# Performance work log

Measured on AMD Instinct MI355X. Metric: run time of the kernel, lower is better.

The kernel has to match this reference:

```python
import jax, jax.numpy as jnp
import numpy as np

N_NODES = 50000
N_EDGES = 800000
NFEAT, NHID, IN_HEAD, NCLASS, OUT_HEAD = 256, 16, 8, 47, 1
NEG_SLOPE = 0.2


def setup_inputs() -> dict:
    key = jax.random.key(0)
    ks = jax.random.split(key, 10)
    x = jax.random.normal(ks[0], (N_NODES, NFEAT), dtype=jnp.float32)
    edge_index = jax.random.randint(ks[1], (2, N_EDGES), 0, N_NODES, dtype=jnp.int64)
    W1 = jax.random.normal(ks[2], (NFEAT, IN_HEAD * NHID), dtype=jnp.float32) * 0.06
    a1_src = jax.random.normal(ks[3], (IN_HEAD, NHID), dtype=jnp.float32) * 0.25
    a1_dst = jax.random.normal(ks[4], (IN_HEAD, NHID), dtype=jnp.float32) * 0.25
    b1 = jax.random.normal(ks[5], (IN_HEAD * NHID,), dtype=jnp.float32) * 0.02
    W2 = jax.random.normal(ks[6], (IN_HEAD * NHID, NCLASS), dtype=jnp.float32) * 0.09
    a2_src = jax.random.normal(ks[7], (OUT_HEAD, NCLASS), dtype=jnp.float32) * 0.15
    a2_dst = jax.random.normal(ks[8], (OUT_HEAD, NCLASS), dtype=jnp.float32) * 0.15
    b2 = jax.random.normal(ks[9], (NCLASS,), dtype=jnp.float32) * 0.02
    return {"x": x, "edge_index": edge_index, "W1": W1, "a1_src": a1_src,
            "a1_dst": a1_dst, "b1": b1, "W2": W2, "a2_src": a2_src,
            "a2_dst": a2_dst, "b2": b2}


def _gat_layer(x, W, a_src, a_dst, b, src, dst, n_nodes, concat):
    # x: [N, F_in]; W: [F_in, H*C]; a_*: [H, C]
    H, C = a_src.shape
    h = (x @ W).reshape(n_nodes, H, C)                        # [N, H, C]
    # per-node partial attention logits, then gather per edge
    s_src = jnp.einsum('nhc,hc->nh', h, a_src)                # [N, H]
    s_dst = jnp.einsum('nhc,hc->nh', h, a_dst)                # [N, H]
    e = jax.nn.leaky_relu(s_src[src] + s_dst[dst], NEG_SLOPE) # [E, H]
    # segment softmax over destination node
    m = jax.ops.segment_max(e, dst, num_segments=n_nodes)     # [N, H]
    ex = jnp.exp(e - m[dst])
    denom = jax.ops.segment_sum(ex, dst, num_segments=n_nodes)
    alpha = ex / (denom[dst] + 1e-16)                         # [E, H]
    # weighted message aggregation (scatter-add)
    msg = alpha[:, :, None] * h[src]                          # [E, H, C]
    out = jax.ops.segment_sum(msg, dst, num_segments=n_nodes) # [N, H, C]
    out = out.reshape(n_nodes, H * C) if concat else out.mean(axis=1)
    return out + b


def reference(x, edge_index, W1, a1_src, a1_dst, b1, W2, a2_src, a2_dst, b2):
    n = x.shape[0]
    # PyG GATConv default: add self-loops
    loops = jnp.arange(n, dtype=edge_index.dtype)
    src = jnp.concatenate([edge_index[0], loops])
    dst = jnp.concatenate([edge_index[1], loops])
    # eval mode: dropout is identity
    h = _gat_layer(x, W1, a1_src, a1_dst, b1, src, dst, n, concat=True)
    h = jax.nn.elu(h)
    out = _gat_layer(h, W2, a2_src, a2_dst, b2, src, dst, n, concat=False)
    return jax.nn.log_softmax(out, axis=1)
```

## Files before the change

### kernel.cpp

```cpp
#include <hip/hip_runtime.h>
#include <hip/hip_fp16.h>

#define N_NODES 50000
#define N_EDGES 800000
#define E2 (N_EDGES + N_NODES)

#define BSHIFT 6
#define BMASK 63
#define NBUCK 782
#define EPB 4096
#define NBLKC 208

typedef _Float16 h8v __attribute__((ext_vector_type(8)));
typedef float f4v __attribute__((ext_vector_type(4)));


__global__ __launch_bounds__(256) void k_hist(const int* __restrict__ ei,
        int* __restrict__ gh, const float* __restrict__ W1, _Float16* __restrict__ W1T) {
    if (blockIdx.x == NBLKC) {
        for (int i = threadIdx.x; i < 128 * 256; i += 256) {
            int c = i >> 8, k = i & 255;
            W1T[i] = (_Float16)W1[k * 128 + c];
        }
        return;
    }
    __shared__ int h[NBUCK];
    int tid = threadIdx.x;
    for (int b = tid; b < NBUCK; b += 256) h[b] = 0;
    __syncthreads();
    int base = blockIdx.x * EPB;
    for (int i = tid; i < EPB; i += 256) {
        int e = base + i;
        if (e < E2) {
            int dst = (e < N_EDGES) ? ei[N_EDGES + e] : (e - N_EDGES);
            atomicAdd(&h[dst >> BSHIFT], 1);
        }
    }
    __syncthreads();
    for (int b = tid; b < NBUCK; b += 256) gh[blockIdx.x * NBUCK + b] = h[b];
}

__global__ __launch_bounds__(256) void k_colscan(int* __restrict__ gh,
                                                 int* __restrict__ tot) {
    int wave = threadIdx.x >> 6, lane = threadIdx.x & 63;
    int b = blockIdx.x * 4 + wave;
    if (b >= NBUCK) return;
    int carry = 0;
    for (int c = 0; c < NBLKC; c += 64) {
        int k = c + lane;
        int v = (k < NBLKC) ? gh[k * NBUCK + b] : 0;
        int x = v;
        #pragma unroll
        for (int o = 1; o < 64; o <<= 1) { int y = __shfl_up(x, o); if (lane >= o) x += y; }
        if (k < NBLKC) gh[k * NBUCK + b] = carry + x - v;
        carry += __shfl(x, 63);
    }
    if (lane == 0) tot[b] = carry;
}

__global__ __launch_bounds__(1024) void k_btot(const int* __restrict__ tot,
        int* __restrict__ boff, const float* __restrict__ W2, float* __restrict__ W2p) {
    int t = threadIdx.x;
    for (int i = t; i < 128 * 48; i += 1024) {
        int k = i / 48, c = i - k * 48;
        W2p[i] = (c < 47) ? W2[k * 47 + c] : 0.f;
    }
    int v = (t < NBUCK) ? tot[t] : 0;
    __shared__ int ws[16];
    int lane = t & 63, w = t >> 6;
    int x = v;
    #pragma unroll
    for (int o = 1; o < 64; o <<= 1) { int y = __shfl_up(x, o); if (lane >= o) x += y; }
    if (lane == 63) ws[w] = x;
    __syncthreads();
    if (t == 0) {
        #pragma unroll
        for (int j = 1; j < 16; ++j) ws[j] += ws[j - 1];
    }
    __syncthreads();
    int add = (w == 0) ? 0 : ws[w - 1];
    int excl = add + x - v;
    if (t < NBUCK) boff[t] = excl;
    if (t == NBUCK - 1) boff[NBUCK] = excl + v;
}

__global__ __launch_bounds__(256) void k_place(const int* __restrict__ ei,
        const int* __restrict__ gh, const int* __restrict__ boff,
        unsigned int* __restrict__ brec) {
    __shared__ int sbase[NBUCK];
    __shared__ int cnt[NBUCK];
    int tid = threadIdx.x;
    for (int b = tid; b < NBUCK; b += 256) {
        sbase[b] = boff[b] + gh[blockIdx.x * NBUCK + b];
        cnt[b] = 0;
    }
    __syncthreads();
    int base = blockIdx.x * EPB;
    for (int i = tid; i < EPB; i += 256) {
        int e = base + i;
        if (e < E2) {
            int src, dst;
            if (e < N_EDGES) { src = ei[e]; dst = ei[N_EDGES + e]; }
            else             { src = dst = e - N_EDGES; }
            int b = dst >> BSHIFT;
            int r = atomicAdd(&cnt[b], 1);
            brec[sbase[b] + r] = ((unsigned int)(dst & BMASK) << 16) | (unsigned int)src;
        }
    }
}

__global__ __launch_bounds__(256) void k_finalize(const unsigned int* __restrict__ brec,
        const int* __restrict__ boff, unsigned short* __restrict__ csr_src,
        int* __restrict__ offs) {
    int B = blockIdx.x;
    int tid = threadIdx.x;
    int base = boff[B];
    int total = boff[B + 1] - base;
    __shared__ int hist[64], cur[64];
    __shared__ unsigned short stage[2048];
    if (tid < 64) hist[tid] = 0;
    __syncthreads();
    const unsigned int* bp = brec + base;
    for (int i = tid; i < total; i += 256) atomicAdd(&hist[bp[i] >> 16], 1);
    __syncthreads();
    if (tid < 64) {
        int v = hist[tid];
        int x = v;
        #pragma unroll
        for (int o = 1; o < 64; o <<= 1) { int y = __shfl_up(x, o); if (tid >= o) x += y; }
        int excl = x - v;
        cur[tid] = excl;
        int n = B * 64 + tid;
        if (n < N_NODES) offs[n] = base + excl;
    }
    if (B == NBUCK - 1 && tid == 0) offs[N_NODES] = boff[NBUCK];
    __syncthreads();
    if (total <= 2048) {
        for (int i = tid; i < total; i += 256) {
            unsigned int r = bp[i];
            int p = atomicAdd(&cur[r >> 16], 1);
            stage[p] = (unsigned short)(r & 0xFFFFu);
        }
        __syncthreads();
        for (int i = tid; i < total; i += 256) csr_src[base + i] = stage[i];
    } else {
        for (int i = tid; i < total; i += 256) {
            unsigned int r = bp[i];
            int p = atomicAdd(&cur[r >> 16], 1);
            csr_src[base + p] = (unsigned short)(r & 0xFFFFu);
        }
    }
}


__global__ __launch_bounds__(128) void k_gemm1(const float* __restrict__ x,
        const _Float16* __restrict__ W1T, _Float16* __restrict__ h1h) {
    int lane = threadIdx.x & 63;
    int wv = threadIdx.x >> 6;
    int rowbase = blockIdx.x * 64 + wv * 32;
    int r0 = lane & 15;
    int kg = lane >> 4;
    f4v acc[2][8];
    #pragma unroll
    for (int i = 0; i < 2; ++i)
        #pragma unroll
        for (int j = 0; j < 8; ++j) acc[i][j] = (f4v)0.f;

    #pragma unroll 1
    for (int kt = 0; kt < 256; kt += 32) {
        h8v a[2];
        #pragma unroll
        for (int rf = 0; rf < 2; ++rf) {
            int row = rowbase + rf * 16 + r0;
            if (row >= N_NODES) row = N_NODES - 1;
            const float* ap = x + (size_t)row * 256 + kt + kg * 8;
            float4 lo = *(const float4*)ap;
            float4 hi = *(const float4*)(ap + 4);
            h8v t;
            t[0] = (_Float16)lo.x; t[1] = (_Float16)lo.y;
            t[2] = (_Float16)lo.z; t[3] = (_Float16)lo.w;
            t[4] = (_Float16)hi.x; t[5] = (_Float16)hi.y;
            t[6] = (_Float16)hi.z; t[7] = (_Float16)hi.w;
            a[rf] = t;
        }
        #pragma unroll
        for (int cf = 0; cf < 8; ++cf) {
            h8v b = *(const h8v*)(W1T + (size_t)(cf * 16 + r0) * 256 + kt + kg * 8);
            acc[0][cf] = __builtin_amdgcn_mfma_f32_16x16x32_f16(a[0], b, acc[0][cf], 0, 0, 0);
            acc[1][cf] = __builtin_amdgcn_mfma_f32_16x16x32_f16(a[1], b, acc[1][cf], 0, 0, 0);
        }
    }
    #pragma unroll
    for (int rf = 0; rf < 2; ++rf) {
        #pragma unroll
        for (int r = 0; r < 4; ++r) {
            int row = rowbase + rf * 16 + kg * 4 + r;
            if (row < N_NODES) {
                _Float16* orow = h1h + (size_t)row * 128 + r0;
                #pragma unroll
                for (int cf = 0; cf < 8; ++cf)
                    orow[cf * 16] = (_Float16)acc[rf][cf][r];
            }
        }
    }
}


__global__ void k_logits1(const __half* __restrict__ h1h,
                          const float* __restrict__ a1s, const float* __restrict__ a1d,
                          float* __restrict__ s1s, float* __restrict__ s1d) {
    int idx = blockIdx.x * blockDim.x + threadIdx.x;
    if (idx >= N_NODES * 8) return;
    int n = idx >> 3, h = idx & 7;
    const __half2* hp2 = (const __half2*)(h1h + (size_t)n * 128 + h * 16);
    float ss = 0.f, sd = 0.f;
    #pragma unroll
    for (int c2 = 0; c2 < 8; ++c2) {
        float2 v = __half22float2(hp2[c2]);
        ss += v.x * a1s[h * 16 + 2 * c2] + v.y * a1s[h * 16 + 2 * c2 + 1];
        sd += v.x * a1d[h * 16 + 2 * c2] + v.y * a1d[h * 16 + 2 * c2 + 1];
    }
    s1s[idx] = ss;
    s1d[idx] = sd;
}


__global__ __launch_bounds__(256) void k_agg1(const __half* __restrict__ h1h,
        const float* __restrict__ s1s, const float* __restrict__ s1d,
        const int* __restrict__ offs, const unsigned short* __restrict__ csr_src,
        const float* __restrict__ b1, __half* __restrict__ h2o) {
    int wave = threadIdx.x >> 6;
    int lane = threadIdx.x & 63;
    int n = blockIdx.x * 4 + wave;
    int beg = offs[n];
    int deg = offs[n + 1] - beg;

    int h = lane & 7;
    int slot = lane >> 3;
    int grp = lane >> 4;
    int cidx = lane & 15;
    int hc = cidx >> 1;
    float sdh = s1d[n * 8 + h];

    float dsum = 0.f;
    float acc[8] = {0.f, 0.f, 0.f, 0.f, 0.f, 0.f, 0.f, 0.f};
    for (int chunk = 0; chunk < deg; chunk += 16) {
        int i0 = chunk + slot;
        int i1 = chunk + 8 + slot;
        int e0 = csr_src[beg + ((i0 < deg) ? i0 : (deg - 1))];
        int e1 = csr_src[beg + ((i1 < deg) ? i1 : (deg - 1))];
        float a0 = 0.f, a1 = 0.f;
        if (i0 < deg) {
            float e = s1s[e0 * 8 + h] + sdh;
            e = (e > 0.f) ? e : 0.2f * e;
            a0 = __expf(e);
            dsum += a0;
        }
        if (i1 < deg) {
            float e = s1s[e1 * 8 + h] + sdh;
            e = (e > 0.f) ? e : 0.2f * e;
            a1 = __expf(e);
            dsum += a1;
        }
        int   s0 = __shfl(e0, grp * 8);       float w0 = __shfl(a0, grp * 8 + hc);
        int   s1 = __shfl(e0, (4 + grp) * 8); float w1 = __shfl(a0, (4 + grp) * 8 + hc);
        int   s2 = __shfl(e1, grp * 8);       float w2 = __shfl(a1, grp * 8 + hc);
        int   s3 = __shfl(e1, (4 + grp) * 8); float w3 = __shfl(a1, (4 + grp) * 8 + hc);
        h8v v0 = *(const h8v*)(h1h + (size_t)s0 * 128 + cidx * 8);
        h8v v1 = *(const h8v*)(h1h + (size_t)s1 * 128 + cidx * 8);
        h8v v2 = *(const h8v*)(h1h + (size_t)s2 * 128 + cidx * 8);
        h8v v3 = *(const h8v*)(h1h + (size_t)s3 * 128 + cidx * 8);
        #pragma unroll
        for (int j = 0; j < 8; ++j) acc[j] += w0 * (float)v0[j];
        #pragma unroll
        for (int j = 0; j < 8; ++j) acc[j] += w1 * (float)v1[j];
        #pragma unroll
        for (int j = 0; j < 8; ++j) acc[j] += w2 * (float)v2[j];
        #pragma unroll
        for (int j = 0; j < 8; ++j) acc[j] += w3 * (float)v3[j];
    }
    dsum += __shfl_xor(dsum, 8);
    dsum += __shfl_xor(dsum, 16);
    dsum += __shfl_xor(dsum, 32);
    float rd = 1.f / __shfl(dsum, hc);
    #pragma unroll
    for (int j = 0; j < 8; ++j) {
        acc[j] += __shfl_xor(acc[j], 16);
        acc[j] += __shfl_xor(acc[j], 32);
    }
    int c0 = cidx * 8 + grp * 2;
    float va = acc[grp * 2] * rd + b1[c0];
    va = (va > 0.f) ? va : (__expf(va) - 1.f);
    float vb = acc[grp * 2 + 1] * rd + b1[c0 + 1];
    vb = (vb > 0.f) ? vb : (__expf(vb) - 1.f);
    *(__half2*)(h2o + (size_t)n * 128 + c0) = __floats2half2_rn(va, vb);
}


__global__ __launch_bounds__(256) void k_gemm2(const __half* __restrict__ h2,
        const float* __restrict__ W2p,
        const float* __restrict__ a2s, const float* __restrict__ a2d,
        __half* __restrict__ g2h, float* __restrict__ s2s, float* __restrict__ s2d) {
    int n = blockIdx.x * 256 + threadIdx.x;
    bool valid = (n < N_NODES);
    int nn = valid ? n : (N_NODES - 1);
    const __half2* hrow = (const __half2*)(h2 + (size_t)nn * 128);
    float4 acc[12];
    #pragma unroll
    for (int j = 0; j < 12; ++j) acc[j] = make_float4(0.f, 0.f, 0.f, 0.f);
    #pragma unroll 1
    for (int k = 0; k < 128; k += 4) {
        float2 h01 = __half22float2(hrow[k / 2]);
        float2 h23 = __half22float2(hrow[k / 2 + 1]);
        float hk[4] = {h01.x, h01.y, h23.x, h23.y};
        #pragma unroll
        for (int kk = 0; kk < 4; ++kk) {
            const float* wrow = W2p + (size_t)(k + kk) * 48;
            #pragma unroll
            for (int j = 0; j < 12; ++j) {
                float4 wv = *(const float4*)(wrow + j * 4);
                acc[j].x += hk[kk] * wv.x;
                acc[j].y += hk[kk] * wv.y;
                acc[j].z += hk[kk] * wv.z;
                acc[j].w += hk[kk] * wv.w;
            }
        }
    }
    float vs = 0.f, vd = 0.f;
    #pragma unroll
    for (int j = 0; j < 12; ++j) {
        int c = j * 4;
        vs += acc[j].x * a2s[c + 0]; vd += acc[j].x * a2d[c + 0];
        vs += acc[j].y * a2s[c + 1]; vd += acc[j].y * a2d[c + 1];
        vs += acc[j].z * a2s[c + 2]; vd += acc[j].z * a2d[c + 2];
        if (j < 11) { vs += acc[j].w * a2s[c + 3]; vd += acc[j].w * a2d[c + 3]; }
    }
    if (valid) {
        __half2* orow = (__half2*)(g2h + (size_t)n * 48);
        #pragma unroll
        for (int j = 0; j < 12; ++j) {
            orow[j * 2 + 0] = __floats2half2_rn(acc[j].x, acc[j].y);
            orow[j * 2 + 1] = __floats2half2_rn(acc[j].z, acc[j].w);
        }
        s2s[n] = vs;
        s2d[n] = vd;
    }
}


__global__ __launch_bounds__(256) void k_agg2(const __half* __restrict__ g2h,
        const float* __restrict__ s2s, const float* __restrict__ s2d,
        const int* __restrict__ offs, const unsigned short* __restrict__ csr_src,
        const float* __restrict__ b2, float* __restrict__ outp) {
    int wave = threadIdx.x >> 6, lane = threadIdx.x & 63;
    int n = blockIdx.x * 4 + wave;
    int beg = offs[n];
    int deg = offs[n + 1] - beg;
    float sdn = s2d[n];
    int c = (lane < 47) ? lane : 47;

    float dsum = 0.f;
    float acc = 0.f;
    for (int chunk = 0; chunk < deg; chunk += 64) {
        int i = chunk + lane;
        int esrc = csr_src[beg + ((i < deg) ? i : (deg - 1))];
        float aN = 0.f;
        if (i < deg) {
            float e = s2s[esrc] + sdn;
            e = (e > 0.f) ? e : 0.2f * e;
            aN = __expf(e);
            dsum += aN;
        }
        int lim = deg - chunk; if (lim > 64) lim = 64;
        for (int g = 0; g < lim; g += 8) {
            int   srcs[8];
            float as[8];
            #pragma unroll
            for (int s = 0; s < 8; ++s) {
                srcs[s] = __shfl(esrc, g + s);
                as[s]   = __shfl(aN, g + s);
            }
            __half v[8];
            #pragma unroll
            for (int s = 0; s < 8; ++s) v[s] = g2h[(size_t)srcs[s] * 48 + c];
            #pragma unroll
            for (int s = 0; s < 8; ++s) acc += as[s] * __half2float(v[s]);
        }
    }
    #pragma unroll
    for (int o = 32; o; o >>= 1) dsum += __shfl_xor(dsum, o);
    acc *= 1.f / dsum;

    float l = (lane < 47) ? acc + b2[lane] : -1e30f;
    float rm = l;
    #pragma unroll
    for (int o = 32; o; o >>= 1) rm = fmaxf(rm, __shfl_xor(rm, o));
    float p = (lane < 47) ? __expf(l - rm) : 0.f;
    float ps = p;
    #pragma unroll
    for (int o = 32; o; o >>= 1) ps += __shfl_xor(ps, o);
    float lse = rm + __logf(ps);
    if (lane < 47) outp[(size_t)n * 47 + lane] = l - lse;
}


extern "C" void kernel_launch(void* const* d_in, const int* in_sizes, int n_in,
                              void* d_out, int out_size, void* d_ws, size_t ws_size,
                              hipStream_t stream) {
    const float* x   = (const float*)d_in[0];
    const int*   ei  = (const int*)d_in[1];
    const float* W1  = (const float*)d_in[2];
    const float* a1s = (const float*)d_in[3];
    const float* a1d = (const float*)d_in[4];
    const float* b1  = (const float*)d_in[5];
    const float* W2  = (const float*)d_in[6];
    const float* a2s = (const float*)d_in[7];
    const float* a2d = (const float*)d_in[8];
    const float* b2  = (const float*)d_in[9];
    float* outp = (float*)d_out;

    char* ws = (char*)d_ws;
    size_t off = 0;
    auto alloc = [&](size_t bytes) -> void* {
        void* p = ws + off;
        off += (bytes + 255) & ~(size_t)255;
        return p;
    };
    int* gh      = (int*)alloc((size_t)NBLKC * NBUCK * 4);
    int* tot     = (int*)alloc((size_t)NBUCK * 4);
    int* boff    = (int*)alloc((size_t)(NBUCK + 1) * 4);
    unsigned int* brec = (unsigned int*)alloc((size_t)E2 * 4);
    unsigned short* csr_src = (unsigned short*)alloc((size_t)E2 * 2);
    int* offs    = (int*)alloc((size_t)(N_NODES + 1) * 4);
    __half* h1h  = (__half*)alloc((size_t)N_NODES * 128 * 2);
    float* s1s   = (float*)alloc((size_t)N_NODES * 8 * 4);
    float* s1d   = (float*)alloc((size_t)N_NODES * 8 * 4);
    __half* h2h  = (__half*)alloc((size_t)N_NODES * 128 * 2);
    __half* g2h  = (__half*)alloc((size_t)N_NODES * 48 * 2);
    float* s2s   = (float*)alloc((size_t)N_NODES * 4);
    float* s2d   = (float*)alloc((size_t)N_NODES * 4);
    float* W2p   = (float*)alloc((size_t)128 * 48 * 4);
    _Float16* W1T = (_Float16*)alloc((size_t)128 * 256 * 2);

    (void)in_sizes; (void)n_in; (void)out_size; (void)ws_size;

    k_hist<<<NBLKC + 1, 256, 0, stream>>>(ei, gh, W1, W1T);
    k_colscan<<<(NBUCK + 3) / 4, 256, 0, stream>>>(gh, tot);
    k_btot<<<1, 1024, 0, stream>>>(tot, boff, W2, W2p);
    k_place<<<NBLKC, 256, 0, stream>>>(ei, gh, boff, brec);
    k_finalize<<<NBUCK, 256, 0, stream>>>(brec, boff, csr_src, offs);

    k_gemm1<<<(N_NODES + 63) / 64, 128, 0, stream>>>(x, W1T, (_Float16*)h1h);
    k_logits1<<<(N_NODES * 8 + 255) / 256, 256, 0, stream>>>(h1h, a1s, a1d, s1s, s1d);
    k_agg1<<<N_NODES / 4, 256, 0, stream>>>(h1h, s1s, s1d, offs, csr_src, b1, h2h);

    k_gemm2<<<(N_NODES + 255) / 256, 256, 0, stream>>>(h2h, W2p, a2s, a2d, g2h, s2s, s2d);
    k_agg2<<<N_NODES / 4, 256, 0, stream>>>(g2h, s2s, s2d, offs, csr_src, b2, outp);
}
```

Baseline: 178.4 us.

## Fuse logits into GEMM1, merge bucket scan kernels, halve edges per histogram block

Computes the layer-1 attention logits inside the GEMM1 epilogue using cross-lane shuffle reductions over the fp32 accumulators, which removes the separate k_logits1 kernel and its re-read of h1h. The bucket-total scan and the W2 padding move into k_colscan's last-arriving block, found with an atomic counter and threadfence, so the 1024-thread k_btot launch goes away. The counting-sort block size is halved (NBLKC doubled), which spreads the histogram and place work over more blocks but doubles the per-block histogram rows the column scan must walk. Logits now come from fp32 accumulators instead of fp16-rounded values, so they differ slightly in precision.

```diff
diff --git a/kernel.cpp b/kernel.cpp
--- a/kernel.cpp
+++ b/kernel.cpp
@@ -8,16 +8,18 @@
 #define BSHIFT 6
 #define BMASK 63
 #define NBUCK 782
-#define EPB 4096
-#define NBLKC 208
+#define EPB 2048
+#define NBLKC 416
 
 typedef _Float16 h8v __attribute__((ext_vector_type(8)));
 typedef float f4v __attribute__((ext_vector_type(4)));
 
 
 __global__ __launch_bounds__(256) void k_hist(const int* __restrict__ ei,
-        int* __restrict__ gh, const float* __restrict__ W1, _Float16* __restrict__ W1T) {
+        int* __restrict__ gh, const float* __restrict__ W1, _Float16* __restrict__ W1T,
+        int* __restrict__ flag) {
     if (blockIdx.x == NBLKC) {
+        if (threadIdx.x == 0) *flag = 0;
         for (int i = threadIdx.x; i < 128 * 256; i += 256) {
             int c = i >> 8, k = i & 255;
             W1T[i] = (_Float16)W1[k * 128 + c];
@@ -41,47 +43,61 @@
 }
 
 __global__ __launch_bounds__(256) void k_colscan(int* __restrict__ gh,
-                                                 int* __restrict__ tot) {
+        int* __restrict__ tot, int* __restrict__ boff, int* __restrict__ flag,
+        const float* __restrict__ W2, float* __restrict__ W2p) {
+    __shared__ int s_last;
+    __shared__ int ws2[4];
     int wave = threadIdx.x >> 6, lane = threadIdx.x & 63;
     int b = blockIdx.x * 4 + wave;
-    if (b >= NBUCK) return;
-    int carry = 0;
-    for (int c = 0; c < NBLKC; c += 64) {
-        int k = c + lane;
-        int v = (k < NBLKC) ? gh[k * NBUCK + b] : 0;
-        int x = v;
-        #pragma unroll
-        for (int o = 1; o < 64; o <<= 1) { int y = __shfl_up(x, o); if (lane >= o) x += y; }
-        if (k < NBLKC) gh[k * NBUCK + b] = carry + x - v;
-        carry += __shfl(x, 63);
-    }
-    if (lane == 0) tot[b] = carry;
-}
-
-__global__ __launch_bounds__(1024) void k_btot(const int* __restrict__ tot,
-        int* __restrict__ boff, const float* __restrict__ W2, float* __restrict__ W2p) {
+    if (b < NBUCK) {
+        int carry = 0;
+        for (int c = 0; c < NBLKC; c += 64) {
+            int k = c + lane;
+            int v = (k < NBLKC) ? gh[k * NBUCK + b] : 0;
+            int x = v;
+            #pragma unroll
+            for (int o = 1; o < 64; o <<= 1) { int y = __shfl_up(x, o); if (lane >= o) x += y; }
+            if (k < NBLKC) gh[k * NBUCK + b] = carry + x - v;
+            carry += __shfl(x, 63);
+        }
+        if (lane == 0) tot[b] = carry;
+    }
+    __syncthreads();
+    if (threadIdx.x == 0) {
+        __threadfence();
+        int prev = atomicAdd(flag, 1);
+        s_last = (prev == (int)gridDim.x - 1) ? 1 : 0;
+    }
+    __syncthreads();
+    if (!s_last) return;
+    __threadfence();
     int t = threadIdx.x;
-    for (int i = t; i < 128 * 48; i += 1024) {
+    for (int i = t; i < 128 * 48; i += 256) {
         int k = i / 48, c = i - k * 48;
         W2p[i] = (c < 47) ? W2[k * 47 + c] : 0.f;
     }
-    int v = (t < NBUCK) ? tot[t] : 0;
-    __shared__ int ws[16];
-    int lane = t & 63, w = t >> 6;
-    int x = v;
+    int v4[4]; int s = 0;
+    #pragma unroll
+    for (int j = 0; j < 4; ++j) {
+        int b2 = t * 4 + j;
+        v4[j] = (b2 < NBUCK) ? tot[b2] : 0;
+        s += v4[j];
+    }
+    int x = s;
     #pragma unroll
     for (int o = 1; o < 64; o <<= 1) { int y = __shfl_up(x, o); if (lane >= o) x += y; }
-    if (lane == 63) ws[w] = x;
-    __syncthreads();
-    if (t == 0) {
-        #pragma unroll
-        for (int j = 1; j < 16; ++j) ws[j] += ws[j - 1];
-    }
-    __syncthreads();
-    int add = (w == 0) ? 0 : ws[w - 1];
-    int excl = add + x - v;
-    if (t < NBUCK) boff[t] = excl;
-    if (t == NBUCK - 1) boff[NBUCK] = excl + v;
+    if (lane == 63) ws2[wave] = x;
+    __syncthreads();
+    int add = 0;
+    for (int j = 0; j < wave; ++j) add += ws2[j];
+    int run = add + x - s;
+    #pragma unroll
+    for (int j = 0; j < 4; ++j) {
+        int b2 = t * 4 + j;
+        if (b2 < NBUCK) boff[b2] = run;
+        run += v4[j];
+    }
+    if (t == 255) boff[NBUCK] = run;
 }
 
 __global__ __launch_bounds__(256) void k_place(const int* __restrict__ ei,
@@ -154,7 +170,9 @@
 
 
 __global__ __launch_bounds__(128) void k_gemm1(const float* __restrict__ x,
-        const _Float16* __restrict__ W1T, _Float16* __restrict__ h1h) {
+        const _Float16* __restrict__ W1T, _Float16* __restrict__ h1h,
+        const float* __restrict__ a1s, const float* __restrict__ a1d,
+        float* __restrict__ s1s, float* __restrict__ s1d) {
     int lane = threadIdx.x & 63;
     int wv = threadIdx.x >> 6;
     int rowbase = blockIdx.x * 64 + wv * 32;
@@ -190,38 +208,47 @@
             acc[1][cf] = __builtin_amdgcn_mfma_f32_16x16x32_f16(a[1], b, acc[1][cf], 0, 0, 0);
         }
     }
+    float a1sv[8], a1dv[8];
+    #pragma unroll
+    for (int cf = 0; cf < 8; ++cf) {
+        a1sv[cf] = a1s[cf * 16 + r0];
+        a1dv[cf] = a1d[cf * 16 + r0];
+    }
     #pragma unroll
     for (int rf = 0; rf < 2; ++rf) {
         #pragma unroll
         for (int r = 0; r < 4; ++r) {
             int row = rowbase + rf * 16 + kg * 4 + r;
+            float ss[8], sd[8];
+            #pragma unroll
+            for (int cf = 0; cf < 8; ++cf) {
+                float av = acc[rf][cf][r];
+                ss[cf] = av * a1sv[cf];
+                sd[cf] = av * a1dv[cf];
+            }
+            #pragma unroll
+            for (int o = 1; o < 16; o <<= 1) {
+                #pragma unroll
+                for (int cf = 0; cf < 8; ++cf) {
+                    ss[cf] += __shfl_xor(ss[cf], o);
+                    sd[cf] += __shfl_xor(sd[cf], o);
+                }
+            }
             if (row < N_NODES) {
                 _Float16* orow = h1h + (size_t)row * 128 + r0;
                 #pragma unroll
                 for (int cf = 0; cf < 8; ++cf)
                     orow[cf * 16] = (_Float16)acc[rf][cf][r];
+                int j = r0 & 7;
+                float outv = 0.f;
+                #pragma unroll
+                for (int q = 0; q < 8; ++q)
+                    if (j == q) outv = (r0 < 8) ? ss[q] : sd[q];
+                if (r0 < 8) s1s[row * 8 + r0] = outv;
+                else        s1d[row * 8 + (r0 - 8)] = outv;
             }
         }
     }
-}
-
-
-__global__ void k_logits1(const __half* __restrict__ h1h,
-                          const float* __restrict__ a1s, const float* __restrict__ a1d,
-                          float* __restrict__ s1s, float* __restrict__ s1d) {
-    int idx = blockIdx.x * blockDim.x + threadIdx.x;
-    if (idx >= N_NODES * 8) return;
-    int n = idx >> 3, h = idx & 7;
-    const __half2* hp2 = (const __half2*)(h1h + (size_t)n * 128 + h * 16);
-    float ss = 0.f, sd = 0.f;
-    #pragma unroll
-    for (int c2 = 0; c2 < 8; ++c2) {
-        float2 v = __half22float2(hp2[c2]);
-        ss += v.x * a1s[h * 16 + 2 * c2] + v.y * a1s[h * 16 + 2 * c2 + 1];
-        sd += v.x * a1d[h * 16 + 2 * c2] + v.y * a1d[h * 16 + 2 * c2 + 1];
-    }
-    s1s[idx] = ss;
-    s1d[idx] = sd;
 }
 
 
@@ -429,6 +456,7 @@
     int* gh      = (int*)alloc((size_t)NBLKC * NBUCK * 4);
     int* tot     = (int*)alloc((size_t)NBUCK * 4);
     int* boff    = (int*)alloc((size_t)(NBUCK + 1) * 4);
+    int* flag    = (int*)alloc(256);
     unsigned int* brec = (unsigned int*)alloc((size_t)E2 * 4);
     unsigned short* csr_src = (unsigned short*)alloc((size_t)E2 * 2);
     int* offs    = (int*)alloc((size_t)(N_NODES + 1) * 4);
@@ -444,14 +472,13 @@
 
     (void)in_sizes; (void)n_in; (void)out_size; (void)ws_size;
 
-    k_hist<<<NBLKC + 1, 256, 0, stream>>>(ei, gh, W1, W1T);
-    k_colscan<<<(NBUCK + 3) / 4, 256, 0, stream>>>(gh, tot);
-    k_btot<<<1, 1024, 0, stream>>>(tot, boff, W2, W2p);
+    k_hist<<<NBLKC + 1, 256, 0, stream>>>(ei, gh, W1, W1T, flag);
+    k_colscan<<<(NBUCK + 3) / 4, 256, 0, stream>>>(gh, tot, boff, flag, W2, W2p);
     k_place<<<NBLKC, 256, 0, stream>>>(ei, gh, boff, brec);
     k_finalize<<<NBUCK, 256, 0, stream>>>(brec, boff, csr_src, offs);
 
-    k_gemm1<<<(N_NODES + 63) / 64, 128, 0, stream>>>(x, W1T, (_Float16*)h1h);
-    k_logits1<<<(N_NODES * 8 + 255) / 256, 256, 0, stream>>>(h1h, a1s, a1d, s1s, s1d);
+    k_gemm1<<<(N_NODES + 63) / 64, 128, 0, stream>>>(x, W1T, (_Float16*)h1h,
+                                                     a1s, a1d, s1s, s1d);
     k_agg1<<<N_NODES / 4, 256, 0, stream>>>(h1h, s1s, s1d, offs, csr_src, b1, h2h);
 
     k_gemm2<<<(N_NODES + 255) / 256, 256, 0, stream>>>(h2h, W2p, a2s, a2d, g2h, s2s, s2d);
```

Result: slower. 197.3 us (median of 2 runs) (+10.6%).
